# Performance work log

Hardware: AMD Instinct MI355X
Metric: run time of the kernel (lower is better)

Reference implementation:

```python
import jax, jax.numpy as jnp
import numpy as np

N, D, C = 12288, 64, 3
K, GAMMA = 85, 0.5
SAMPLE = 2000


def _safe_sqrt(sq):
    # sqrt with zero gradient at exactly-zero inputs (matches torch cdist/norm backward)
    sq = jnp.maximum(sq, 0.0)
    return jnp.where(sq > 0, jnp.sqrt(jnp.where(sq > 0, sq, 1.0)), 0.0)


def _cdist(a, b):
    # pairwise euclidean distances [Na, Nb]
    sq = jnp.sum(a * a, -1)[:, None] + jnp.sum(b * b, -1)[None, :] - 2.0 * (a @ b.T)
    return _safe_sqrt(sq)


def setup_inputs() -> dict:
    key = jax.random.key(0)
    k1, k2 = jax.random.split(key)
    return {
        "embeddings": jax.random.normal(k1, (N, D), dtype=jnp.float32),
        "coords": jax.random.normal(k2, (N, C), dtype=jnp.float32),
    }


def reference(embeddings, coords):
    n = embeddings.shape[0]
    sample_size = min(n, SAMPLE)
    # deterministic stand-in for torch.randperm sampling
    idx = jax.random.permutation(jax.random.key(42), n)[:sample_size]
    emb_s = embeddings[idx]
    coord_s = coords[idx]

    # Pearson correlation between flattened sample distance matrices
    ed = _cdist(emb_s, emb_s).ravel()
    cd = _cdist(coord_s, coord_s).ravel()
    ec = ed - ed.mean()
    cc = cd - cd.mean()
    es = jnp.sqrt((ec * ec).mean() + 1e-8)
    cs = jnp.sqrt((cc * cc).mean() + 1e-8)
    pearson = (ec * cc).mean() / (es * cs + 1e-8)
    pearson_loss = 1.0 - pearson

    k = min(K, n - 1)
    # KNN in coordinate space, no grad (torch.no_grad)
    coords_ng = jax.lax.stop_gradient(coords)
    full = _cdist(coords_ng, coords_ng)               # [N, N]
    _, knn_idx = jax.lax.top_k(-full, k + 1)          # smallest distances
    knn_idx = knn_idx[:, 1:]                          # drop self -> [N, k]

    nb_emb = embeddings[knn_idx]                      # [N, k, D]
    nb_coord = coords[knn_idx]                        # [N, k, C]
    pred_dist = _safe_sqrt(jnp.sum((embeddings[:, None, :] - nb_emb) ** 2, -1))  # [N, k]
    true_dist = _safe_sqrt(jnp.sum((coords[:, None, :] - nb_coord) ** 2, -1))    # [N, k]
    decay_weight = jnp.exp(-GAMMA * true_dist)
    local_loss = jnp.mean((pred_dist - true_dist) ** 2 * decay_weight)

    return pearson_loss + 0.5 * local_loss
```

## Files before the change

### kernel.cpp

```cpp
#include <hip/hip_runtime.h>
#include <math.h>

#define NPTS 12288
#define DIM 64
#define KNN 85
#define KSEL 86
#define SAMPLE 2000
#define SSTRIDE 6
#define GAMMA 0.5f
#define NT 256
#define WPB 4
#define VIT 12
#define NV 48
#define VCAP 256
#define PT 64
#define PPITCH 68
#define PBLK 1024


struct PearsonS {
  float EpT[DIM][PPITCH];
  float EqT[DIM][PPITCH];
  float Cp[PT][4];
  float Cq[PT][4];
  float np_[PT];
  float nq_[PT];
  double wred[4][5];
};
struct KnnS {
  unsigned h[256];
  unsigned bmax[WPB];
  unsigned long long vkey[VCAP];
  unsigned long long thrkey;
  unsigned vcnt;
};
union SharedU { PearsonS p; KnnS k; };

__global__ void prep_kernel(const float* __restrict__ coord,
                            float* __restrict__ cx, float* __restrict__ cy,
                            float* __restrict__ cz) {
  int j = blockIdx.x * 256 + threadIdx.x;
  if (j < NPTS) {
    cx[j] = coord[3 * j];
    cy[j] = coord[3 * j + 1];
    cz[j] = coord[3 * j + 2];
  }
}

__device__ __forceinline__ void pearson_body(
    SharedU& sh, const float* __restrict__ emb, const float* __restrict__ coord,
    double* __restrict__ acc) {
  const int tid = threadIdx.x;
  const int tx = tid & 15, ty = tid >> 4;
  const int lane = tid & 63, wv = tid >> 6;
  const int pb = blockIdx.x;
  const int p0 = (pb >> 5) * PT, q0 = (pb & 31) * PT;

  for (int e = tid; e < PT * DIM; e += 256) {
    int r = e >> 6, k = e & 63;
    int gp = (p0 + r < SAMPLE ? p0 + r : 0) * SSTRIDE;
    int gq = (q0 + r < SAMPLE ? q0 + r : 0) * SSTRIDE;
    sh.p.EpT[k][r] = emb[(size_t)gp * DIM + k];
    sh.p.EqT[k][r] = emb[(size_t)gq * DIM + k];
  }
  if (tid < PT) {
    int g = (p0 + tid < SAMPLE ? p0 + tid : 0) * SSTRIDE;
    sh.p.Cp[tid][0] = coord[3 * g]; sh.p.Cp[tid][1] = coord[3 * g + 1]; sh.p.Cp[tid][2] = coord[3 * g + 2];
  } else if (tid < 2 * PT) {
    int r = tid - PT;
    int g = (q0 + r < SAMPLE ? q0 + r : 0) * SSTRIDE;
    sh.p.Cq[r][0] = coord[3 * g]; sh.p.Cq[r][1] = coord[3 * g + 1]; sh.p.Cq[r][2] = coord[3 * g + 2];
  }
  __syncthreads();

  if (tid < PT) {
    float a = 0.f;
    #pragma unroll 8
    for (int k = 0; k < DIM; ++k) { float v = sh.p.EpT[k][tid]; a += v * v; }
    sh.p.np_[tid] = a;
  } else if (tid < 2 * PT) {
    int r = tid - PT;
    float a = 0.f;
    #pragma unroll 8
    for (int k = 0; k < DIM; ++k) { float v = sh.p.EqT[k][r]; a += v * v; }
    sh.p.nq_[r] = a;
  }
  __syncthreads();

  float s[4][4] = {};
  #pragma unroll 8
  for (int k = 0; k < DIM; ++k) {
    float4 ep = *(const float4*)&sh.p.EpT[k][4 * ty];
    float4 eq = *(const float4*)&sh.p.EqT[k][4 * tx];
    float pa[4] = { ep.x, ep.y, ep.z, ep.w };
    float qa[4] = { eq.x, eq.y, eq.z, eq.w };
    #pragma unroll
    for (int a = 0; a < 4; ++a)
      #pragma unroll
      for (int b = 0; b < 4; ++b)
        s[a][b] += pa[a] * qa[b];
  }

  const float npr[4] = { sh.p.np_[4 * ty], sh.p.np_[4 * ty + 1], sh.p.np_[4 * ty + 2], sh.p.np_[4 * ty + 3] };
  const float nqr[4] = { sh.p.nq_[4 * tx], sh.p.nq_[4 * tx + 1], sh.p.nq_[4 * tx + 2], sh.p.nq_[4 * tx + 3] };

  double se = 0, sc = 0, se2 = 0, sc2 = 0, sec = 0;
  #pragma unroll
  for (int a = 0; a < 4; ++a)
    #pragma unroll
    for (int b = 0; b < 4; ++b) {
      int p = p0 + 4 * ty + a, q = q0 + 4 * tx + b;
      if (p < SAMPLE && q < SAMPLE) {
        float sq = fmaxf(npr[a] + nqr[b] - 2.f * s[a][b], 0.f);
        float ed = sqrtf(sq);
        float dx = sh.p.Cp[4 * ty + a][0] - sh.p.Cq[4 * tx + b][0];
        float dy = sh.p.Cp[4 * ty + a][1] - sh.p.Cq[4 * tx + b][1];
        float dz = sh.p.Cp[4 * ty + a][2] - sh.p.Cq[4 * tx + b][2];
        float cd = sqrtf(fmaxf(dx * dx + dy * dy + dz * dz, 0.f));
        se += (double)ed; sc += (double)cd;
        se2 += (double)ed * ed; sc2 += (double)cd * cd;
        sec += (double)ed * cd;
      }
    }

  double vals[5] = { se, sc, se2, sc2, sec };
  #pragma unroll
  for (int v = 0; v < 5; ++v) {
    #pragma unroll
    for (int off = 32; off > 0; off >>= 1) vals[v] += __shfl_xor(vals[v], off, 64);
  }
  if (lane == 0) {
    #pragma unroll
    for (int v = 0; v < 5; ++v) sh.p.wred[wv][v] = vals[v];
  }
  __syncthreads();
  if (tid < 5) {
    double sm = sh.p.wred[0][tid] + sh.p.wred[1][tid] + sh.p.wred[2][tid] + sh.p.wred[3][tid];
    atomicAdd(&acc[tid], sm);
  }
}

__device__ __forceinline__ void knn_body(
    SharedU& sh, const float* __restrict__ emb, const float* __restrict__ cx,
    const float* __restrict__ cy, const float* __restrict__ cz,
    double* __restrict__ acc) {
  const int i = blockIdx.x - PBLK;
  const int tid = threadIdx.x;
  const int lane = tid & 63;
  const int wv = tid >> 6;

  const float qx = cx[i], qy = cy[i], qz = cz[i];
  const float4* CX4 = (const float4*)cx;
  const float4* CY4 = (const float4*)cy;
  const float4* CZ4 = (const float4*)cz;

  unsigned d2b[NV];
  #pragma unroll
  for (int it = 0; it < VIT; ++it) {
    int idx = it * NT + tid;
    float4 x4 = CX4[idx], y4 = CY4[idx], z4 = CZ4[idx];
    float dx, dy, dz;
    dx = qx - x4.x; dy = qy - y4.x; dz = qz - z4.x;
    d2b[4 * it + 0] = __float_as_uint(dx * dx + dy * dy + dz * dz);
    dx = qx - x4.y; dy = qy - y4.y; dz = qz - z4.y;
    d2b[4 * it + 1] = __float_as_uint(dx * dx + dy * dy + dz * dz);
    dx = qx - x4.z; dy = qy - y4.z; dz = qz - z4.z;
    d2b[4 * it + 2] = __float_as_uint(dx * dx + dy * dy + dz * dz);
    dx = qx - x4.w; dy = qy - y4.w; dz = qz - z4.w;
    d2b[4 * it + 3] = __float_as_uint(dx * dx + dy * dy + dz * dz);
  }
  const float4 ei4 = ((const float4*)(emb + (size_t)i * DIM))[lane & 15];

  unsigned m1 = 0xFFFFFFFFu, m2 = 0xFFFFFFFFu;
  #pragma unroll
  for (int t = 0; t < NV; ++t) {
    unsigned u = d2b[t];
    unsigned hi = u > m1 ? u : m1;
    m1 = u < m1 ? u : m1;
    m2 = hi < m2 ? hi : m2;
  }
  unsigned M2w = m2;
  #pragma unroll
  for (int off = 32; off > 0; off >>= 1) {
    unsigned t2 = __shfl_xor((int)M2w, off, 64);
    M2w = t2 > M2w ? t2 : M2w;
  }
  if (lane == 0) sh.k.bmax[wv] = M2w;
  sh.k.h[tid] = 0;
  if (tid == 0) { sh.k.vcnt = 0; sh.k.thrkey = 0xFFFFFFFFFFFFFFFFULL; }
  __syncthreads();

  const unsigned b0 = sh.k.bmax[0], b1 = sh.k.bmax[1];
  const unsigned b2_ = sh.k.bmax[2], b3 = sh.k.bmax[3];
  unsigned Bu = b0 < b1 ? b0 : b1;
  unsigned Bu2 = b2_ < b3 ? b2_ : b3;
  Bu = Bu < Bu2 ? Bu : Bu2;
  const float Bf = fmaxf(__uint_as_float(Bu), 1e-30f);
  const float sbin = 256.0f / Bf;

  #pragma unroll
  for (int t = 0; t < NV; ++t) {
    unsigned u = d2b[t];
    if (u <= Bu) {
      int bb = (int)(__uint_as_float(u) * sbin);
      bb = bb > 255 ? 255 : bb;
      atomicAdd(&sh.k.h[bb], 1u);
    }
  }
  __syncthreads();

  unsigned c0 = sh.k.h[4 * lane], c1 = sh.k.h[4 * lane + 1];
  unsigned c2 = sh.k.h[4 * lane + 2], c3 = sh.k.h[4 * lane + 3];
  unsigned lt = c0 + c1 + c2 + c3;
  unsigned incl = lt;
  #pragma unroll
  for (int off = 1; off < 64; off <<= 1) {
    unsigned t2 = __shfl_up(incl, off, 64);
    if (lane >= off) incl += t2;
  }
  unsigned excl = incl - lt;
  bool has = (lt > 0) && (excl < KSEL) && (KSEL <= incl);
  unsigned bin = 4 * lane, cum = excl;
  if (cum + c0 >= KSEL) { bin = 4 * lane; }
  else { cum += c0;
    if (cum + c1 >= KSEL) { bin = 4 * lane + 1; }
    else { cum += c1;
      if (cum + c2 >= KSEL) { bin = 4 * lane + 2; }
      else { bin = 4 * lane + 3; } } }
  unsigned long long bal = __ballot(has);
  int src = __ffsll((unsigned long long)bal) - 1;
  unsigned bsel = __shfl((int)bin, src, 64);
  float Uf = (float)(bsel + 1) * (Bf * (1.0f / 256.0f)) * 1.000002f;
  const unsigned T = __float_as_uint(Uf);

  #pragma unroll
  for (int t = 0; t < NV; ++t) {
    unsigned u = d2b[t];
    if (u <= T) {
      unsigned pos = atomicAdd(&sh.k.vcnt, 1u);
      if (pos < VCAP) {
        unsigned pj = (unsigned)(4 * ((t >> 2) * NT + tid) + (t & 3));
        sh.k.vkey[pos] = ((unsigned long long)u << 14) | pj;
      }
    }
  }
  __syncthreads();
  const unsigned vc = sh.k.vcnt;
  const int tot = (int)(vc < VCAP ? vc : VCAP);

  if (tid < tot) {
    const unsigned long long kt = sh.k.vkey[tid];
    int rank = 0;
    for (int k = 0; k < tot; ++k) rank += (sh.k.vkey[k] < kt) ? 1 : 0;
    if (rank == KSEL - 1) sh.k.thrkey = kt;
  }
  __syncthreads();
  const unsigned long long thr64 = sh.k.thrkey;

  const int q = lane >> 4;
  const int l16 = lane & 15;
  float lsum = 0.f;
  for (int base = wv * 4; base < tot; base += 16) {
    int idx = base + q;
    bool valid = false;
    unsigned u = 0; int j = 0;
    if (idx < tot) {
      unsigned long long kk64 = sh.k.vkey[idx];
      u = (unsigned)(kk64 >> 14);
      j = (int)(kk64 & 0x3FFFu);
      valid = (kk64 <= thr64) && (j != i);
    }
    float s = 0.f;
    if (valid) {
      float4 e4 = ((const float4*)(emb + (size_t)j * DIM))[l16];
      float d0 = ei4.x - e4.x, d1 = ei4.y - e4.y;
      float d2 = ei4.z - e4.z, d3 = ei4.w - e4.w;
      s = d0 * d0 + d1 * d1 + d2 * d2 + d3 * d3;
    }
    s += __shfl_xor(s, 1, 64);
    s += __shfl_xor(s, 2, 64);
    s += __shfl_xor(s, 4, 64);
    s += __shfl_xor(s, 8, 64);
    if (valid && l16 == 0) {
      float td = sqrtf(__uint_as_float(u));
      float pd = sqrtf(fmaxf(s, 0.f));
      float diff = pd - td;
      lsum += diff * diff * expf(-GAMMA * td);
    }
  }
  #pragma unroll
  for (int off = 32; off > 0; off >>= 1) lsum += __shfl_xor(lsum, off, 64);
  if (lane == 0) atomicAdd(&acc[5 + (i & 7) * 4 + wv], (double)lsum);
}

__global__ __launch_bounds__(NT) void fused_kernel(
    const float* __restrict__ emb, const float* __restrict__ coord,
    const float* __restrict__ cx, const float* __restrict__ cy,
    const float* __restrict__ cz, double* __restrict__ acc) {
  __shared__ SharedU sh;
  if (blockIdx.x < PBLK) {
    pearson_body(sh, emb, coord, acc);
  } else {
    knn_body(sh, emb, cx, cy, cz, acc);
  }
}

__global__ void finalize_kernel(const double* __restrict__ acc,
                                float* __restrict__ out) {
  double M = (double)SAMPLE * (double)SAMPLE;
  double med = acc[0] / M, mcd = acc[1] / M;
  double ve = acc[2] / M - med * med;
  double vc = acc[3] / M - mcd * mcd;
  double es = sqrt(ve + 1e-8);
  double cs = sqrt(vc + 1e-8);
  double cov = acc[4] / M - med * mcd;
  double pearson = cov / (es * cs + 1e-8);
  double lsum = 0.0;
  for (int s = 5; s < 37; ++s) lsum += acc[s];
  double local = lsum / ((double)NPTS * (double)KNN);
  out[0] = (float)((1.0 - pearson) + 0.5 * local);
}

extern "C" void kernel_launch(void* const* d_in, const int* in_sizes, int n_in,
                              void* d_out, int out_size, void* d_ws, size_t ws_size,
                              hipStream_t stream) {
  const float* emb = (const float*)d_in[0];
  const float* coord = (const float*)d_in[1];
  double* acc = (double*)d_ws;
  float* cx = (float*)((char*)d_ws + 512);
  float* cy = cx + NPTS;
  float* cz = cy + NPTS;

  hipMemsetAsync(d_ws, 0, 37 * sizeof(double), stream);

  prep_kernel<<<(NPTS + 255) / 256, 256, 0, stream>>>(coord, cx, cy, cz);

  fused_kernel<<<PBLK + NPTS, NT, 0, stream>>>(emb, coord, cx, cy, cz, acc);

  finalize_kernel<<<1, 1, 0, stream>>>(acc, (float*)d_out);
}
```

Baseline: 327.7 us.

## Process two KNN query points per block to reuse coordinate loads

Each KNN block now handles two query points, so every float4 coordinate load is shared by both distance computations. This halves the KNN grid and its global coordinate traffic, and it interleaves the histogram, selection and ranking steps for the two queries between the same barriers. In exchange it doubles register usage for the distance arrays (96 per thread), which may lower occupancy, and each block now runs both queries' rank and neighbor loops one after the other.

```diff
diff --git a/kernel.cpp b/kernel.cpp
--- a/kernel.cpp
+++ b/kernel.cpp
@@ -10,6 +10,8 @@
 #define GAMMA 0.5f
 #define NT 256
 #define WPB 4
+#define QPB 2
+#define KBLK (NPTS / QPB)
 #define VIT 12
 #define NV 48
 #define VCAP 256
@@ -25,14 +27,14 @@
   float Cq[PT][4];
   float np_[PT];
   float nq_[PT];
-  double wred[4][5];
+  double wred[WPB][5];
 };
 struct KnnS {
-  unsigned h[256];
-  unsigned bmax[WPB];
-  unsigned long long vkey[VCAP];
-  unsigned long long thrkey;
-  unsigned vcnt;
+  unsigned hA[256], hB[256];
+  unsigned bmaxA[WPB], bmaxB[WPB];
+  unsigned long long vkeyA[VCAP], vkeyB[VCAP];
+  unsigned long long thrkeyA, thrkeyB;
+  unsigned vcntA, vcntB;
 };
 union SharedU { PearsonS p; KnnS k; };
 
@@ -140,141 +142,199 @@
   }
 }
 
+
 __device__ __forceinline__ void knn_body(
     SharedU& sh, const float* __restrict__ emb, const float* __restrict__ cx,
     const float* __restrict__ cy, const float* __restrict__ cz,
     double* __restrict__ acc) {
-  const int i = blockIdx.x - PBLK;
+  const int i0 = QPB * (blockIdx.x - PBLK);
+  const int i1 = i0 + 1;
   const int tid = threadIdx.x;
   const int lane = tid & 63;
   const int wv = tid >> 6;
 
-  const float qx = cx[i], qy = cy[i], qz = cz[i];
+  const float qxA = cx[i0], qyA = cy[i0], qzA = cz[i0];
+  const float qxB = cx[i1], qyB = cy[i1], qzB = cz[i1];
   const float4* CX4 = (const float4*)cx;
   const float4* CY4 = (const float4*)cy;
   const float4* CZ4 = (const float4*)cz;
 
-  unsigned d2b[NV];
+  unsigned dA[NV], dB[NV];
+  unsigned m1A = 0xFFFFFFFFu, m2A = 0xFFFFFFFFu;
+  unsigned m1B = 0xFFFFFFFFu, m2B = 0xFFFFFFFFu;
   #pragma unroll
   for (int it = 0; it < VIT; ++it) {
     int idx = it * NT + tid;
     float4 x4 = CX4[idx], y4 = CY4[idx], z4 = CZ4[idx];
-    float dx, dy, dz;
-    dx = qx - x4.x; dy = qy - y4.x; dz = qz - z4.x;
-    d2b[4 * it + 0] = __float_as_uint(dx * dx + dy * dy + dz * dz);
-    dx = qx - x4.y; dy = qy - y4.y; dz = qz - z4.y;
-    d2b[4 * it + 1] = __float_as_uint(dx * dx + dy * dy + dz * dz);
-    dx = qx - x4.z; dy = qy - y4.z; dz = qz - z4.z;
-    d2b[4 * it + 2] = __float_as_uint(dx * dx + dy * dy + dz * dz);
-    dx = qx - x4.w; dy = qy - y4.w; dz = qz - z4.w;
-    d2b[4 * it + 3] = __float_as_uint(dx * dx + dy * dy + dz * dz);
-  }
-  const float4 ei4 = ((const float4*)(emb + (size_t)i * DIM))[lane & 15];
-
-  unsigned m1 = 0xFFFFFFFFu, m2 = 0xFFFFFFFFu;
+    float px[4] = { x4.x, x4.y, x4.z, x4.w };
+    float py[4] = { y4.x, y4.y, y4.z, y4.w };
+    float pz[4] = { z4.x, z4.y, z4.z, z4.w };
+    #pragma unroll
+    for (int c = 0; c < 4; ++c) {
+      float dxA = qxA - px[c], dyA = qyA - py[c], dzA = qzA - pz[c];
+      unsigned uA = __float_as_uint(dxA * dxA + dyA * dyA + dzA * dzA);
+      dA[4 * it + c] = uA;
+      unsigned hiA = uA > m1A ? uA : m1A;
+      m1A = uA < m1A ? uA : m1A;
+      m2A = hiA < m2A ? hiA : m2A;
+      float dxB = qxB - px[c], dyB = qyB - py[c], dzB = qzB - pz[c];
+      unsigned uB = __float_as_uint(dxB * dxB + dyB * dyB + dzB * dzB);
+      dB[4 * it + c] = uB;
+      unsigned hiB = uB > m1B ? uB : m1B;
+      m1B = uB < m1B ? uB : m1B;
+      m2B = hiB < m2B ? hiB : m2B;
+    }
+  }
+
+  unsigned MA = m2A, MB = m2B;
+  #pragma unroll
+  for (int off = 32; off > 0; off >>= 1) {
+    unsigned tA = __shfl_xor((int)MA, off, 64);
+    MA = tA > MA ? tA : MA;
+    unsigned tB = __shfl_xor((int)MB, off, 64);
+    MB = tB > MB ? tB : MB;
+  }
+  if (lane == 0) { sh.k.bmaxA[wv] = MA; sh.k.bmaxB[wv] = MB; }
+  sh.k.hA[tid] = 0; sh.k.hB[tid] = 0;
+  if (tid == 0) {
+    sh.k.vcntA = 0; sh.k.vcntB = 0;
+    sh.k.thrkeyA = 0xFFFFFFFFFFFFFFFFULL;
+    sh.k.thrkeyB = 0xFFFFFFFFFFFFFFFFULL;
+  }
+  __syncthreads();
+
+  unsigned BuA = sh.k.bmaxA[0], BuB = sh.k.bmaxB[0];
+  #pragma unroll
+  for (int w = 1; w < WPB; ++w) {
+    unsigned a = sh.k.bmaxA[w]; BuA = a < BuA ? a : BuA;
+    unsigned b = sh.k.bmaxB[w]; BuB = b < BuB ? b : BuB;
+  }
+  const float BfA = fmaxf(__uint_as_float(BuA), 1e-30f);
+  const float BfB = fmaxf(__uint_as_float(BuB), 1e-30f);
+  const float sbA = 256.0f / BfA;
+  const float sbB = 256.0f / BfB;
+
   #pragma unroll
   for (int t = 0; t < NV; ++t) {
-    unsigned u = d2b[t];
-    unsigned hi = u > m1 ? u : m1;
-    m1 = u < m1 ? u : m1;
-    m2 = hi < m2 ? hi : m2;
-  }
-  unsigned M2w = m2;
-  #pragma unroll
-  for (int off = 32; off > 0; off >>= 1) {
-    unsigned t2 = __shfl_xor((int)M2w, off, 64);
-    M2w = t2 > M2w ? t2 : M2w;
-  }
-  if (lane == 0) sh.k.bmax[wv] = M2w;
-  sh.k.h[tid] = 0;
-  if (tid == 0) { sh.k.vcnt = 0; sh.k.thrkey = 0xFFFFFFFFFFFFFFFFULL; }
-  __syncthreads();
-
-  const unsigned b0 = sh.k.bmax[0], b1 = sh.k.bmax[1];
-  const unsigned b2_ = sh.k.bmax[2], b3 = sh.k.bmax[3];
-  unsigned Bu = b0 < b1 ? b0 : b1;
-  unsigned Bu2 = b2_ < b3 ? b2_ : b3;
-  Bu = Bu < Bu2 ? Bu : Bu2;
-  const float Bf = fmaxf(__uint_as_float(Bu), 1e-30f);
-  const float sbin = 256.0f / Bf;
+    unsigned uA = dA[t];
+    if (uA <= BuA) {
+      int bb = (int)(__uint_as_float(uA) * sbA);
+      bb = bb > 255 ? 255 : bb;
+      atomicAdd(&sh.k.hA[bb], 1u);
+    }
+    unsigned uB = dB[t];
+    if (uB <= BuB) {
+      int bb = (int)(__uint_as_float(uB) * sbB);
+      bb = bb > 255 ? 255 : bb;
+      atomicAdd(&sh.k.hB[bb], 1u);
+    }
+  }
+  __syncthreads();
+
+  unsigned TA, TB;
+  {
+    unsigned c0 = sh.k.hA[4 * lane], c1 = sh.k.hA[4 * lane + 1];
+    unsigned c2 = sh.k.hA[4 * lane + 2], c3 = sh.k.hA[4 * lane + 3];
+    unsigned lt = c0 + c1 + c2 + c3;
+    unsigned incl = lt;
+    #pragma unroll
+    for (int off = 1; off < 64; off <<= 1) {
+      unsigned t2 = __shfl_up(incl, off, 64);
+      if (lane >= off) incl += t2;
+    }
+    unsigned excl = incl - lt;
+    bool has = (lt > 0) && (excl < KSEL) && (KSEL <= incl);
+    unsigned bin = 4 * lane, cum = excl;
+    if (cum + c0 >= KSEL) { bin = 4 * lane; }
+    else { cum += c0;
+      if (cum + c1 >= KSEL) { bin = 4 * lane + 1; }
+      else { cum += c1;
+        if (cum + c2 >= KSEL) { bin = 4 * lane + 2; }
+        else { bin = 4 * lane + 3; } } }
+    unsigned long long bal = __ballot(has);
+    int src = __ffsll((unsigned long long)bal) - 1;
+    unsigned bsel = __shfl((int)bin, src, 64);
+    TA = __float_as_uint((float)(bsel + 1) * (BfA * (1.0f / 256.0f)) * 1.000002f);
+  }
+  {
+    unsigned c0 = sh.k.hB[4 * lane], c1 = sh.k.hB[4 * lane + 1];
+    unsigned c2 = sh.k.hB[4 * lane + 2], c3 = sh.k.hB[4 * lane + 3];
+    unsigned lt = c0 + c1 + c2 + c3;
+    unsigned incl = lt;
+    #pragma unroll
+    for (int off = 1; off < 64; off <<= 1) {
+      unsigned t2 = __shfl_up(incl, off, 64);
+      if (lane >= off) incl += t2;
+    }
+    unsigned excl = incl - lt;
+    bool has = (lt > 0) && (excl < KSEL) && (KSEL <= incl);
+    unsigned bin = 4 * lane, cum = excl;
+    if (cum + c0 >= KSEL) { bin = 4 * lane; }
+    else { cum += c0;
+      if (cum + c1 >= KSEL) { bin = 4 * lane + 1; }
+      else { cum += c1;
+        if (cum + c2 >= KSEL) { bin = 4 * lane + 2; }
+        else { bin = 4 * lane + 3; } } }
+    unsigned long long bal = __ballot(has);
+    int src = __ffsll((unsigned long long)bal) - 1;
+    unsigned bsel = __shfl((int)bin, src, 64);
+    TB = __float_as_uint((float)(bsel + 1) * (BfB * (1.0f / 256.0f)) * 1.000002f);
+  }
 
   #pragma unroll
   for (int t = 0; t < NV; ++t) {
-    unsigned u = d2b[t];
-    if (u <= Bu) {
-      int bb = (int)(__uint_as_float(u) * sbin);
-      bb = bb > 255 ? 255 : bb;
-      atomicAdd(&sh.k.h[bb], 1u);
-    }
-  }
-  __syncthreads();
-
-  unsigned c0 = sh.k.h[4 * lane], c1 = sh.k.h[4 * lane + 1];
-  unsigned c2 = sh.k.h[4 * lane + 2], c3 = sh.k.h[4 * lane + 3];
-  unsigned lt = c0 + c1 + c2 + c3;
-  unsigned incl = lt;
-  #pragma unroll
-  for (int off = 1; off < 64; off <<= 1) {
-    unsigned t2 = __shfl_up(incl, off, 64);
-    if (lane >= off) incl += t2;
-  }
-  unsigned excl = incl - lt;
-  bool has = (lt > 0) && (excl < KSEL) && (KSEL <= incl);
-  unsigned bin = 4 * lane, cum = excl;
-  if (cum + c0 >= KSEL) { bin = 4 * lane; }
-  else { cum += c0;
-    if (cum + c1 >= KSEL) { bin = 4 * lane + 1; }
-    else { cum += c1;
-      if (cum + c2 >= KSEL) { bin = 4 * lane + 2; }
-      else { bin = 4 * lane + 3; } } }
-  unsigned long long bal = __ballot(has);
-  int src = __ffsll((unsigned long long)bal) - 1;
-  unsigned bsel = __shfl((int)bin, src, 64);
-  float Uf = (float)(bsel + 1) * (Bf * (1.0f / 256.0f)) * 1.000002f;
-  const unsigned T = __float_as_uint(Uf);
-
-  #pragma unroll
-  for (int t = 0; t < NV; ++t) {
-    unsigned u = d2b[t];
-    if (u <= T) {
-      unsigned pos = atomicAdd(&sh.k.vcnt, 1u);
-      if (pos < VCAP) {
-        unsigned pj = (unsigned)(4 * ((t >> 2) * NT + tid) + (t & 3));
-        sh.k.vkey[pos] = ((unsigned long long)u << 14) | pj;
-      }
-    }
-  }
-  __syncthreads();
-  const unsigned vc = sh.k.vcnt;
-  const int tot = (int)(vc < VCAP ? vc : VCAP);
-
-  if (tid < tot) {
-    const unsigned long long kt = sh.k.vkey[tid];
+    unsigned pj = (unsigned)(4 * ((t >> 2) * NT + tid) + (t & 3));
+    unsigned uA = dA[t];
+    if (uA <= TA) {
+      unsigned pos = atomicAdd(&sh.k.vcntA, 1u);
+      if (pos < VCAP) sh.k.vkeyA[pos] = ((unsigned long long)uA << 14) | pj;
+    }
+    unsigned uB = dB[t];
+    if (uB <= TB) {
+      unsigned pos = atomicAdd(&sh.k.vcntB, 1u);
+      if (pos < VCAP) sh.k.vkeyB[pos] = ((unsigned long long)uB << 14) | pj;
+    }
+  }
+  const float4 eiA = ((const float4*)(emb + (size_t)i0 * DIM))[lane & 15];
+  const float4 eiB = ((const float4*)(emb + (size_t)i1 * DIM))[lane & 15];
+  __syncthreads();
+  const int totA = (int)(sh.k.vcntA < VCAP ? sh.k.vcntA : VCAP);
+  const int totB = (int)(sh.k.vcntB < VCAP ? sh.k.vcntB : VCAP);
+
+  if (tid < totA) {
+    const unsigned long long kt = sh.k.vkeyA[tid];
     int rank = 0;
-    for (int k = 0; k < tot; ++k) rank += (sh.k.vkey[k] < kt) ? 1 : 0;
-    if (rank == KSEL - 1) sh.k.thrkey = kt;
-  }
-  __syncthreads();
-  const unsigned long long thr64 = sh.k.thrkey;
+    for (int k = 0; k < totA; ++k) rank += (sh.k.vkeyA[k] < kt) ? 1 : 0;
+    if (rank == KSEL - 1) sh.k.thrkeyA = kt;
+  }
+  if (tid < totB) {
+    const unsigned long long kt = sh.k.vkeyB[tid];
+    int rank = 0;
+    for (int k = 0; k < totB; ++k) rank += (sh.k.vkeyB[k] < kt) ? 1 : 0;
+    if (rank == KSEL - 1) sh.k.thrkeyB = kt;
+  }
+  __syncthreads();
+  const unsigned long long thrA = sh.k.thrkeyA;
+  const unsigned long long thrB = sh.k.thrkeyB;
 
   const int q = lane >> 4;
   const int l16 = lane & 15;
-  float lsum = 0.f;
-  for (int base = wv * 4; base < tot; base += 16) {
+  float lsumA = 0.f, lsumB = 0.f;
+  for (int base = wv * 4; base < totA; base += 16) {
     int idx = base + q;
     bool valid = false;
     unsigned u = 0; int j = 0;
-    if (idx < tot) {
-      unsigned long long kk64 = sh.k.vkey[idx];
-      u = (unsigned)(kk64 >> 14);
-      j = (int)(kk64 & 0x3FFFu);
-      valid = (kk64 <= thr64) && (j != i);
+    if (idx < totA) {
+      unsigned long long kk = sh.k.vkeyA[idx];
+      u = (unsigned)(kk >> 14);
+      j = (int)(kk & 0x3FFFu);
+      valid = (kk <= thrA) && (j != i0);
     }
     float s = 0.f;
     if (valid) {
       float4 e4 = ((const float4*)(emb + (size_t)j * DIM))[l16];
-      float d0 = ei4.x - e4.x, d1 = ei4.y - e4.y;
-      float d2 = ei4.z - e4.z, d3 = ei4.w - e4.w;
+      float d0 = eiA.x - e4.x, d1 = eiA.y - e4.y;
+      float d2 = eiA.z - e4.z, d3 = eiA.w - e4.w;
       s = d0 * d0 + d1 * d1 + d2 * d2 + d3 * d3;
     }
     s += __shfl_xor(s, 1, 64);
@@ -285,12 +345,46 @@
       float td = sqrtf(__uint_as_float(u));
       float pd = sqrtf(fmaxf(s, 0.f));
       float diff = pd - td;
-      lsum += diff * diff * expf(-GAMMA * td);
-    }
-  }
-  #pragma unroll
-  for (int off = 32; off > 0; off >>= 1) lsum += __shfl_xor(lsum, off, 64);
-  if (lane == 0) atomicAdd(&acc[5 + (i & 7) * 4 + wv], (double)lsum);
+      lsumA += diff * diff * expf(-GAMMA * td);
+    }
+  }
+  for (int base = wv * 4; base < totB; base += 16) {
+    int idx = base + q;
+    bool valid = false;
+    unsigned u = 0; int j = 0;
+    if (idx < totB) {
+      unsigned long long kk = sh.k.vkeyB[idx];
+      u = (unsigned)(kk >> 14);
+      j = (int)(kk & 0x3FFFu);
+      valid = (kk <= thrB) && (j != i1);
+    }
+    float s = 0.f;
+    if (valid) {
+      float4 e4 = ((const float4*)(emb + (size_t)j * DIM))[l16];
+      float d0 = eiB.x - e4.x, d1 = eiB.y - e4.y;
+      float d2 = eiB.z - e4.z, d3 = eiB.w - e4.w;
+      s = d0 * d0 + d1 * d1 + d2 * d2 + d3 * d3;
+    }
+    s += __shfl_xor(s, 1, 64);
+    s += __shfl_xor(s, 2, 64);
+    s += __shfl_xor(s, 4, 64);
+    s += __shfl_xor(s, 8, 64);
+    if (valid && l16 == 0) {
+      float td = sqrtf(__uint_as_float(u));
+      float pd = sqrtf(fmaxf(s, 0.f));
+      float diff = pd - td;
+      lsumB += diff * diff * expf(-GAMMA * td);
+    }
+  }
+  #pragma unroll
+  for (int off = 32; off > 0; off >>= 1) {
+    lsumA += __shfl_xor(lsumA, off, 64);
+    lsumB += __shfl_xor(lsumB, off, 64);
+  }
+  if (lane == 0) {
+    atomicAdd(&acc[5 + (i0 & 7) * 4 + wv], (double)lsumA);
+    atomicAdd(&acc[5 + (i1 & 7) * 4 + wv], (double)lsumB);
+  }
 }
 
 __global__ __launch_bounds__(NT) void fused_kernel(
@@ -335,7 +429,7 @@
 
   prep_kernel<<<(NPTS + 255) / 256, 256, 0, stream>>>(coord, cx, cy, cz);
 
-  fused_kernel<<<PBLK + NPTS, NT, 0, stream>>>(emb, coord, cx, cy, cz, acc);
+  fused_kernel<<<PBLK + KBLK, NT, 0, stream>>>(emb, coord, cx, cy, cz, acc);
 
   finalize_kernel<<<1, 1, 0, stream>>>(acc, (float*)d_out);
 }
```

After: 408.7 us. +24.7%, slower.

## Make fused kernel persistent: each block runs Pearson tile then twelve KNN queries

Applied to the files above, without the earlier changes.

The launch drops from one block per KNN query plus the Pearson tiles to 1024 blocks. Each block computes one Pearson tile and then loops over twelve KNN queries, reusing its shared memory, which cuts block launch and scheduling overhead. The rank-selection loop is also unrolled by eight, with padded shared storage, and the neighbour-embedding loop issues two gathers per iteration to expose more memory-level parallelism. In exchange, each block now processes its queries serially, there is less oversubscription to hide latency, and correctness depends on proper barriers between successive queries that share the same shared memory.

```diff
diff --git a/kernel.cpp b/kernel.cpp
--- a/kernel.cpp
+++ b/kernel.cpp
@@ -16,6 +16,7 @@
 #define PT 64
 #define PPITCH 68
 #define PBLK 1024
+#define QPB_P (NPTS / PBLK)
 
 
 struct PearsonS {
@@ -25,12 +26,12 @@
   float Cq[PT][4];
   float np_[PT];
   float nq_[PT];
-  double wred[4][5];
+  double wred[WPB][5];
 };
 struct KnnS {
   unsigned h[256];
   unsigned bmax[WPB];
-  unsigned long long vkey[VCAP];
+  unsigned long long vkey[VCAP + 8];
   unsigned long long thrkey;
   unsigned vcnt;
 };
@@ -48,12 +49,11 @@
 }
 
 __device__ __forceinline__ void pearson_body(
-    SharedU& sh, const float* __restrict__ emb, const float* __restrict__ coord,
-    double* __restrict__ acc) {
+    SharedU& sh, int pb, const float* __restrict__ emb,
+    const float* __restrict__ coord, double* __restrict__ acc) {
   const int tid = threadIdx.x;
   const int tx = tid & 15, ty = tid >> 4;
   const int lane = tid & 63, wv = tid >> 6;
-  const int pb = blockIdx.x;
   const int p0 = (pb >> 5) * PT, q0 = (pb & 31) * PT;
 
   for (int e = tid; e < PT * DIM; e += 256) {
@@ -140,11 +140,10 @@
   }
 }
 
-__device__ __forceinline__ void knn_body(
-    SharedU& sh, const float* __restrict__ emb, const float* __restrict__ cx,
-    const float* __restrict__ cy, const float* __restrict__ cz,
-    double* __restrict__ acc) {
-  const int i = blockIdx.x - PBLK;
+__device__ __forceinline__ void knn_one(
+    SharedU& sh, int i, const float* __restrict__ emb,
+    const float* __restrict__ cx, const float* __restrict__ cy,
+    const float* __restrict__ cz, double* __restrict__ acc) {
   const int tid = threadIdx.x;
   const int lane = tid & 63;
   const int wv = tid >> 6;
@@ -251,7 +250,15 @@
   if (tid < tot) {
     const unsigned long long kt = sh.k.vkey[tid];
     int rank = 0;
-    for (int k = 0; k < tot; ++k) rank += (sh.k.vkey[k] < kt) ? 1 : 0;
+    const int lim = (tot + 7) & ~7;
+    for (int k = 0; k < lim; k += 8) {
+      #pragma unroll
+      for (int e = 0; e < 8; ++e) {
+        int kk = k + e;
+        unsigned long long v = sh.k.vkey[kk];
+        rank += (kk < tot && v < kt) ? 1 : 0;
+      }
+    }
     if (rank == KSEL - 1) sh.k.thrkey = kt;
   }
   __syncthreads();
@@ -260,32 +267,40 @@
   const int q = lane >> 4;
   const int l16 = lane & 15;
   float lsum = 0.f;
-  for (int base = wv * 4; base < tot; base += 16) {
-    int idx = base + q;
-    bool valid = false;
-    unsigned u = 0; int j = 0;
-    if (idx < tot) {
-      unsigned long long kk64 = sh.k.vkey[idx];
-      u = (unsigned)(kk64 >> 14);
-      j = (int)(kk64 & 0x3FFFu);
-      valid = (kk64 <= thr64) && (j != i);
-    }
-    float s = 0.f;
-    if (valid) {
-      float4 e4 = ((const float4*)(emb + (size_t)j * DIM))[l16];
-      float d0 = ei4.x - e4.x, d1 = ei4.y - e4.y;
-      float d2 = ei4.z - e4.z, d3 = ei4.w - e4.w;
-      s = d0 * d0 + d1 * d1 + d2 * d2 + d3 * d3;
-    }
-    s += __shfl_xor(s, 1, 64);
-    s += __shfl_xor(s, 2, 64);
-    s += __shfl_xor(s, 4, 64);
-    s += __shfl_xor(s, 8, 64);
-    if (valid && l16 == 0) {
-      float td = sqrtf(__uint_as_float(u));
-      float pd = sqrtf(fmaxf(s, 0.f));
-      float diff = pd - td;
-      lsum += diff * diff * expf(-GAMMA * td);
+  for (int base = wv * 8; base < tot; base += 32) {
+    const int idxs[2] = { base + q, base + 4 + q };
+    bool valid[2]; unsigned uu[2]; int jj[2]; float4 e4v[2];
+    #pragma unroll
+    for (int z = 0; z < 2; ++z) {
+      int idx = idxs[z];
+      valid[z] = false; uu[z] = 0; jj[z] = 0;
+      if (idx < tot) {
+        unsigned long long kk64 = sh.k.vkey[idx];
+        uu[z] = (unsigned)(kk64 >> 14);
+        jj[z] = (int)(kk64 & 0x3FFFu);
+        valid[z] = (kk64 <= thr64) && (jj[z] != i);
+      }
+      e4v[z] = valid[z] ? ((const float4*)(emb + (size_t)jj[z] * DIM))[l16]
+                        : make_float4(0.f, 0.f, 0.f, 0.f);
+    }
+    #pragma unroll
+    for (int z = 0; z < 2; ++z) {
+      float s = 0.f;
+      if (valid[z]) {
+        float d0 = ei4.x - e4v[z].x, d1 = ei4.y - e4v[z].y;
+        float d2 = ei4.z - e4v[z].z, d3 = ei4.w - e4v[z].w;
+        s = d0 * d0 + d1 * d1 + d2 * d2 + d3 * d3;
+      }
+      s += __shfl_xor(s, 1, 64);
+      s += __shfl_xor(s, 2, 64);
+      s += __shfl_xor(s, 4, 64);
+      s += __shfl_xor(s, 8, 64);
+      if (valid[z] && l16 == 0) {
+        float td = sqrtf(__uint_as_float(uu[z]));
+        float pd = sqrtf(fmaxf(s, 0.f));
+        float diff = pd - td;
+        lsum += diff * diff * expf(-GAMMA * td);
+      }
     }
   }
   #pragma unroll
@@ -298,11 +313,11 @@
     const float* __restrict__ cx, const float* __restrict__ cy,
     const float* __restrict__ cz, double* __restrict__ acc) {
   __shared__ SharedU sh;
-  if (blockIdx.x < PBLK) {
-    pearson_body(sh, emb, coord, acc);
-  } else {
-    knn_body(sh, emb, cx, cy, cz, acc);
-  }
+  pearson_body(sh, blockIdx.x, emb, coord, acc);
+  __syncthreads();
+  const int iq0 = blockIdx.x * QPB_P;
+  for (int qq = 0; qq < QPB_P; ++qq)
+    knn_one(sh, iq0 + qq, emb, cx, cy, cz, acc);
 }
 
 __global__ void finalize_kernel(const double* __restrict__ acc,
@@ -335,7 +350,7 @@
 
   prep_kernel<<<(NPTS + 255) / 256, 256, 0, stream>>>(coord, cx, cy, cz);
 
-  fused_kernel<<<PBLK + NPTS, NT, 0, stream>>>(emb, coord, cx, cy, cz, acc);
+  fused_kernel<<<PBLK, NT, 0, stream>>>(emb, coord, cx, cy, cz, acc);
 
   finalize_kernel<<<1, 1, 0, stream>>>(acc, (float*)d_out);
 }
```

Result: slower. 656.1 us (+100.2%).

## Pack KNN distances to 16-bit keys and read Pearson P rows from global memory

Applied to the files above, without the earlier changes.

The KNN path now stores truncated 16-bit float distance keys, two per register, which halves the per-thread distance array. It fuses the min-2 scan into the distance loop and bins the histogram on the truncated keys. Candidates in the selected bin are recomputed at full precision from global coordinates before the exact ranking. The Pearson path drops the shared EpT tile: it reads P rows directly from global memory and computes both norm sets from global float4 loads. This lowers shared memory and register pressure, at the cost of extra global reads and coarser histogram binning that may admit more candidates.

```diff
diff --git a/kernel.cpp b/kernel.cpp
--- a/kernel.cpp
+++ b/kernel.cpp
@@ -19,13 +19,12 @@
 
 
 struct PearsonS {
-  float EpT[DIM][PPITCH];
   float EqT[DIM][PPITCH];
   float Cp[PT][4];
   float Cq[PT][4];
   float np_[PT];
   float nq_[PT];
-  double wred[4][5];
+  double wred[WPB][5];
 };
 struct KnnS {
   unsigned h[256];
@@ -58,41 +57,51 @@
 
   for (int e = tid; e < PT * DIM; e += 256) {
     int r = e >> 6, k = e & 63;
-    int gp = (p0 + r < SAMPLE ? p0 + r : 0) * SSTRIDE;
     int gq = (q0 + r < SAMPLE ? q0 + r : 0) * SSTRIDE;
-    sh.p.EpT[k][r] = emb[(size_t)gp * DIM + k];
     sh.p.EqT[k][r] = emb[(size_t)gq * DIM + k];
   }
   if (tid < PT) {
     int g = (p0 + tid < SAMPLE ? p0 + tid : 0) * SSTRIDE;
     sh.p.Cp[tid][0] = coord[3 * g]; sh.p.Cp[tid][1] = coord[3 * g + 1]; sh.p.Cp[tid][2] = coord[3 * g + 2];
+    const float4* E4 = (const float4*)(emb + (size_t)g * DIM);
+    float a = 0.f;
+    #pragma unroll
+    for (int k4 = 0; k4 < DIM / 4; ++k4) {
+      float4 v = E4[k4];
+      a += v.x * v.x; a += v.y * v.y; a += v.z * v.z; a += v.w * v.w;
+    }
+    sh.p.np_[tid] = a;
   } else if (tid < 2 * PT) {
     int r = tid - PT;
     int g = (q0 + r < SAMPLE ? q0 + r : 0) * SSTRIDE;
     sh.p.Cq[r][0] = coord[3 * g]; sh.p.Cq[r][1] = coord[3 * g + 1]; sh.p.Cq[r][2] = coord[3 * g + 2];
-  }
-  __syncthreads();
-
-  if (tid < PT) {
+    const float4* E4 = (const float4*)(emb + (size_t)g * DIM);
     float a = 0.f;
-    #pragma unroll 8
-    for (int k = 0; k < DIM; ++k) { float v = sh.p.EpT[k][tid]; a += v * v; }
-    sh.p.np_[tid] = a;
-  } else if (tid < 2 * PT) {
-    int r = tid - PT;
-    float a = 0.f;
-    #pragma unroll 8
-    for (int k = 0; k < DIM; ++k) { float v = sh.p.EqT[k][r]; a += v * v; }
+    #pragma unroll
+    for (int k4 = 0; k4 < DIM / 4; ++k4) {
+      float4 v = E4[k4];
+      a += v.x * v.x; a += v.y * v.y; a += v.z * v.z; a += v.w * v.w;
+    }
     sh.p.nq_[r] = a;
   }
   __syncthreads();
 
+  const float* rp0; const float* rp1; const float* rp2; const float* rp3;
+  {
+    int r0 = p0 + 4 * ty;
+    int g0 = (r0     < SAMPLE ? r0     : 0) * SSTRIDE;
+    int g1 = (r0 + 1 < SAMPLE ? r0 + 1 : 0) * SSTRIDE;
+    int g2 = (r0 + 2 < SAMPLE ? r0 + 2 : 0) * SSTRIDE;
+    int g3 = (r0 + 3 < SAMPLE ? r0 + 3 : 0) * SSTRIDE;
+    rp0 = emb + (size_t)g0 * DIM; rp1 = emb + (size_t)g1 * DIM;
+    rp2 = emb + (size_t)g2 * DIM; rp3 = emb + (size_t)g3 * DIM;
+  }
+
   float s[4][4] = {};
-  #pragma unroll 8
+  #pragma unroll 16
   for (int k = 0; k < DIM; ++k) {
-    float4 ep = *(const float4*)&sh.p.EpT[k][4 * ty];
     float4 eq = *(const float4*)&sh.p.EqT[k][4 * tx];
-    float pa[4] = { ep.x, ep.y, ep.z, ep.w };
+    float pa[4] = { rp0[k], rp1[k], rp2[k], rp3[k] };
     float qa[4] = { eq.x, eq.y, eq.z, eq.w };
     #pragma unroll
     for (int a = 0; a < 4; ++a)
@@ -154,36 +163,36 @@
   const float4* CY4 = (const float4*)cy;
   const float4* CZ4 = (const float4*)cz;
 
-  unsigned d2b[NV];
+  unsigned dp[NV / 2];
+  unsigned m1 = 0xFFFFu, m2 = 0xFFFFu;
   #pragma unroll
   for (int it = 0; it < VIT; ++it) {
     int idx = it * NT + tid;
     float4 x4 = CX4[idx], y4 = CY4[idx], z4 = CZ4[idx];
     float dx, dy, dz;
     dx = qx - x4.x; dy = qy - y4.x; dz = qz - z4.x;
-    d2b[4 * it + 0] = __float_as_uint(dx * dx + dy * dy + dz * dz);
+    unsigned t0 = __float_as_uint(dx * dx + dy * dy + dz * dz) >> 16;
     dx = qx - x4.y; dy = qy - y4.y; dz = qz - z4.y;
-    d2b[4 * it + 1] = __float_as_uint(dx * dx + dy * dy + dz * dz);
+    unsigned t1 = __float_as_uint(dx * dx + dy * dy + dz * dz) >> 16;
     dx = qx - x4.z; dy = qy - y4.z; dz = qz - z4.z;
-    d2b[4 * it + 2] = __float_as_uint(dx * dx + dy * dy + dz * dz);
+    unsigned t2 = __float_as_uint(dx * dx + dy * dy + dz * dz) >> 16;
     dx = qx - x4.w; dy = qy - y4.w; dz = qz - z4.w;
-    d2b[4 * it + 3] = __float_as_uint(dx * dx + dy * dy + dz * dz);
+    unsigned t3 = __float_as_uint(dx * dx + dy * dy + dz * dz) >> 16;
+    dp[2 * it]     = t0 | (t1 << 16);
+    dp[2 * it + 1] = t2 | (t3 << 16);
+    unsigned hi;
+    hi = t0 > m1 ? t0 : m1; m1 = t0 < m1 ? t0 : m1; m2 = hi < m2 ? hi : m2;
+    hi = t1 > m1 ? t1 : m1; m1 = t1 < m1 ? t1 : m1; m2 = hi < m2 ? hi : m2;
+    hi = t2 > m1 ? t2 : m1; m1 = t2 < m1 ? t2 : m1; m2 = hi < m2 ? hi : m2;
+    hi = t3 > m1 ? t3 : m1; m1 = t3 < m1 ? t3 : m1; m2 = hi < m2 ? hi : m2;
   }
   const float4 ei4 = ((const float4*)(emb + (size_t)i * DIM))[lane & 15];
 
-  unsigned m1 = 0xFFFFFFFFu, m2 = 0xFFFFFFFFu;
-  #pragma unroll
-  for (int t = 0; t < NV; ++t) {
-    unsigned u = d2b[t];
-    unsigned hi = u > m1 ? u : m1;
-    m1 = u < m1 ? u : m1;
-    m2 = hi < m2 ? hi : m2;
-  }
   unsigned M2w = m2;
   #pragma unroll
   for (int off = 32; off > 0; off >>= 1) {
-    unsigned t2 = __shfl_xor((int)M2w, off, 64);
-    M2w = t2 > M2w ? t2 : M2w;
+    unsigned t2_ = __shfl_xor((int)M2w, off, 64);
+    M2w = t2_ > M2w ? t2_ : M2w;
   }
   if (lane == 0) sh.k.bmax[wv] = M2w;
   sh.k.h[tid] = 0;
@@ -195,16 +204,19 @@
   unsigned Bu = b0 < b1 ? b0 : b1;
   unsigned Bu2 = b2_ < b3 ? b2_ : b3;
   Bu = Bu < Bu2 ? Bu : Bu2;
-  const float Bf = fmaxf(__uint_as_float(Bu), 1e-30f);
-  const float sbin = 256.0f / Bf;
-
-  #pragma unroll
-  for (int t = 0; t < NV; ++t) {
-    unsigned u = d2b[t];
-    if (u <= Bu) {
-      int bb = (int)(__uint_as_float(u) * sbin);
-      bb = bb > 255 ? 255 : bb;
-      atomicAdd(&sh.k.h[bb], 1u);
+  const float sbin = 256.0f / (float)(Bu + 1);
+
+  #pragma unroll
+  for (int t2i = 0; t2i < NV / 2; ++t2i) {
+    unsigned pk = dp[t2i];
+    unsigned ua = pk & 0xFFFFu, ub = pk >> 16;
+    if (ua <= Bu) {
+      int bb = (int)((float)ua * sbin);
+      atomicAdd(&sh.k.h[bb > 255 ? 255 : bb], 1u);
+    }
+    if (ub <= Bu) {
+      int bb = (int)((float)ub * sbin);
+      atomicAdd(&sh.k.h[bb > 255 ? 255 : bb], 1u);
     }
   }
   __syncthreads();
@@ -215,8 +227,8 @@
   unsigned incl = lt;
   #pragma unroll
   for (int off = 1; off < 64; off <<= 1) {
-    unsigned t2 = __shfl_up(incl, off, 64);
-    if (lane >= off) incl += t2;
+    unsigned t2_ = __shfl_up(incl, off, 64);
+    if (lane >= off) incl += t2_;
   }
   unsigned excl = incl - lt;
   bool has = (lt > 0) && (excl < KSEL) && (KSEL <= incl);
@@ -229,19 +241,20 @@
       else { bin = 4 * lane + 3; } } }
   unsigned long long bal = __ballot(has);
   int src = __ffsll((unsigned long long)bal) - 1;
-  unsigned bsel = __shfl((int)bin, src, 64);
-  float Uf = (float)(bsel + 1) * (Bf * (1.0f / 256.0f)) * 1.000002f;
-  const unsigned T = __float_as_uint(Uf);
+  const unsigned bsel = (unsigned)__shfl((int)bin, src, 64);
 
   #pragma unroll
   for (int t = 0; t < NV; ++t) {
-    unsigned u = d2b[t];
-    if (u <= T) {
+    unsigned pk = dp[t >> 1];
+    unsigned ut = (t & 1) ? (pk >> 16) : (pk & 0xFFFFu);
+    int bb = (int)((float)ut * sbin);
+    if (bb <= (int)bsel) {
+      int j = 4 * ((t >> 2) * NT + tid) + (t & 3);
+      float dx = qx - cx[j], dy = qy - cy[j], dz = qz - cz[j];
+      unsigned u = __float_as_uint(dx * dx + dy * dy + dz * dz);
       unsigned pos = atomicAdd(&sh.k.vcnt, 1u);
-      if (pos < VCAP) {
-        unsigned pj = (unsigned)(4 * ((t >> 2) * NT + tid) + (t & 3));
-        sh.k.vkey[pos] = ((unsigned long long)u << 14) | pj;
-      }
+      if (pos < VCAP)
+        sh.k.vkey[pos] = ((unsigned long long)u << 14) | (unsigned)j;
     }
   }
   __syncthreads();
```

Result: no change. 330.1 us (+0.7%).
